# Performance work log

Measured on AMD Instinct MI355X. Metric: run time of the kernel, lower is better.

## Reference

```python
import jax, jax.numpy as jnp
import numpy as np

N = 1024      # n_nodes
S = 32        # state_dim
M = 32        # message_dim
STEPS = 5     # n_steps


def setup_inputs() -> dict:
    key = jax.random.key(0)
    ks = jax.random.split(key, 12)
    w = lambda k, shape: jax.random.normal(k, shape, jnp.float32) * 0.02
    return {
        "J": jax.random.normal(ks[0], (N, N), jnp.float32),
        "b": jax.random.normal(ks[1], (N,), jnp.float32),
        # message_passing MLP (Linear(2S+3->M), Linear(M->M), Linear(M->M))
        "W1": w(ks[2], (M, 2 * S + 3)), "b1": jnp.zeros((M,), jnp.float32),
        "W2": w(ks[3], (M, M)),         "b2": jnp.zeros((M,), jnp.float32),
        "W3": w(ks[4], (M, M)),         "b3": jnp.zeros((M,), jnp.float32),
        # GRU(input=S+M, hidden=S). h0 is always zero in the original forward,
        # so weight_hh never contributes (only bias_hh does) and is omitted.
        "W_ih": w(ks[5], (3 * S, S + M)),
        "b_ih": w(ks[6], (3 * S,)),
        "b_hh": w(ks[7], (3 * S,)),
        # readout MLP (Linear(S->M), Linear(M->M), Linear(M->2))
        "R1": w(ks[8], (M, S)),  "rb1": jnp.zeros((M,), jnp.float32),
        "R2": w(ks[9], (M, M)),  "rb2": jnp.zeros((M,), jnp.float32),
        "R3": w(ks[10], (2, M)), "rb3": jnp.zeros((2,), jnp.float32),
    }


def reference(J, b, W1, b1, W2, b2, W3, b3, W_ih, b_ih, b_hh, R1, rb1, R2, rb2, R3, rb3):
    # Split first linear over the concat [h_i, h_j, J_ij, b_i, b_j] so the
    # [N, N, 2S+3] concat tensor is never materialized.
    W1a, W1b = W1[:, :S], W1[:, S:2 * S]
    wJ, wbi, wbj = W1[:, 2 * S], W1[:, 2 * S + 1], W1[:, 2 * S + 2]

    def step(h, _):
        hi = h @ W1a.T                       # [N, M] (sender part)
        hj = h @ W1b.T                       # [N, M] (receiver part)
        pre = (hi[:, None, :] + hj[None, :, :]
               + J[:, :, None] * wJ
               + b[:, None, None] * wbi
               + b[None, :, None] * wbj
               + b1)                          # [N, N, M]
        x = jax.nn.relu(pre)
        x = jax.nn.relu(x @ W2.T + b2)
        x = jax.nn.relu(x @ W3.T + b3)       # message_i_j: [N, N, M]
        m = x.sum(0)                          # message to node j: sum over senders i
        # GRU with zero initial hidden state: h' = (1-z) * n_gate
        gi = jnp.concatenate([h, m], axis=-1) @ W_ih.T + b_ih  # [N, 3S]
        r = jax.nn.sigmoid(gi[:, :S] + b_hh[:S])
        z = jax.nn.sigmoid(gi[:, S:2 * S] + b_hh[S:2 * S])
        n = jnp.tanh(gi[:, 2 * S:] + r * b_hh[2 * S:])
        return (1.0 - z) * n, None

    h0 = jnp.zeros((N, S), J.dtype)
    h, _ = jax.lax.scan(step, h0, None, length=STEPS)

    r = jax.nn.relu(h @ R1.T + rb1)
    r = jax.nn.relu(r @ R2.T + rb2)
    r = jax.nn.relu(r @ R3.T + rb3)          # [N, 2]
    return jax.nn.sigmoid(r)
```

## Files before the change

### kernel.cpp

```cpp
#include <hip/hip_runtime.h>
#include <math.h>

#define NN 1024

typedef __attribute__((ext_vector_type(8))) short bf16x8;
typedef __attribute__((ext_vector_type(4))) float f32x4;
typedef __attribute__((ext_vector_type(2))) float f32x2;
typedef __attribute__((ext_vector_type(4))) unsigned int u32x4;

__device__ __forceinline__ float sigmoidf_(float x) { return 1.0f / (1.0f + __expf(-x)); }

__device__ __forceinline__ unsigned int pk2(float a, float b) {
    return __builtin_amdgcn_perm(__float_as_uint(a) + 0x8000u,
                                 __float_as_uint(b) + 0x8000u, 0x03020706u);
}
__device__ __forceinline__ unsigned int pkcvt(float a, float b) {
#if __has_builtin(__builtin_amdgcn_cvt_pk_bf16_f32)
    return __builtin_bit_cast(unsigned int, __builtin_amdgcn_cvt_pk_bf16_f32(a, b));
#else
    return pk2(a, b);
#endif
}
__device__ __forceinline__ unsigned short f2bf_rne(float a) {
    unsigned int ua = __float_as_uint(a);
    ua += 0x7fffu + ((ua >> 16) & 1u);
    return (unsigned short)(ua >> 16);
}

#define CFG_FLOATS 2560

__global__ __launch_bounds__(256) void k_pre(
    const float* __restrict__ J, const float* __restrict__ b,
    const float* __restrict__ W1, const float* __restrict__ b1,
    const float* __restrict__ W2, const float* __restrict__ b2,
    const float* __restrict__ W3, const float* __restrict__ b3,
    float* __restrict__ Jt, float* __restrict__ h,
    float* __restrict__ u0, float* __restrict__ v, float* __restrict__ cfg)
{
    __shared__ float tile[32][33];
    const int t = blockIdx.x;
    const int tid = threadIdx.x;
    if (t < 1024) {
        int tx = (t & 31) * 32, ty = (t >> 5) * 32;
        int x = tid & 31, y = tid >> 5;
#pragma unroll
        for (int r = 0; r < 4; r++)
            tile[y + 8 * r][x] = J[(size_t)(ty + y + 8 * r) * NN + tx + x];
        __syncthreads();
#pragma unroll
        for (int r = 0; r < 4; r++)
            Jt[(size_t)(tx + y + 8 * r) * NN + ty + x] = tile[x][y + 8 * r];
    } else if (t < 1152) {
        int idx = (t - 1024) * 256 + tid;
        int row = idx >> 5, mm = idx & 31;
        float bi = b[row];
        h[idx]  = 0.f;
        u0[idx] = bi * W1[mm * 67 + 65];
        v[idx]  = fmaf(bi, W1[mm * 67 + 66], b1[mm]);
    } else if (tid < 64) {
        const int l = tid, p = l & 15, q = l >> 4;
        union FU { unsigned int d[4]; unsigned short s[8]; } t0, t1, t2, t3;
        float wj[8];
#pragma unroll
        for (int jj = 0; jj < 8; jj++) {
            int k = q * 8 + jj;
            t0.s[jj] = f2bf_rne(W2[p * 32 + k]);
            t1.s[jj] = f2bf_rne(W2[(16 + p) * 32 + k]);
            t2.s[jj] = f2bf_rne(W3[p * 32 + k]);
            t3.s[jj] = f2bf_rne(W3[(16 + p) * 32 + k]);
            wj[jj] = W1[k * 67 + 64];
        }
        u32x4* cw = (u32x4*)cfg;
        cw[l]       = *(u32x4*)t0.d;
        cw[64 + l]  = *(u32x4*)t1.d;
        cw[128 + l] = *(u32x4*)t2.d;
        cw[192 + l] = *(u32x4*)t3.d;
        f32x4* cf = (f32x4*)(cfg + 1024);
        f32x4 v0, v1, v2, v3;
#pragma unroll
        for (int r = 0; r < 4; r++) {
            v0[r] = b2[q * 4 + r];  v1[r] = b2[16 + q * 4 + r];
            v2[r] = b3[q * 4 + r];  v3[r] = b3[16 + q * 4 + r];
        }
        cf[l] = v0; cf[64 + l] = v1; cf[128 + l] = v2; cf[192 + l] = v3;
        f32x4* cj = (f32x4*)(cfg + 2048);
        f32x4 wlo, whi;
#pragma unroll
        for (int r = 0; r < 4; r++) { wlo[r] = wj[r]; whi[r] = wj[4 + r]; }
        cj[l] = wlo; cj[64 + l] = whi;
    }
}

__device__ __forceinline__ void tile_body(
    float jw, const float4& ua_c, const float4& ub_c,
    const f32x2* vv2, const f32x2* wj2,
    const bf16x8& w2a0, const bf16x8& w2a1,
    const bf16x8& w3a0, const bf16x8& w3a1,
    const f32x4& b2v0, const f32x4& b2v1,
    const f32x4& b3v0, const f32x4& b3v1,
    int s0, int s1, bool qlo, f32x4& acc0, f32x4& acc1)
{
    const f32x2 jw2 = {jw, jw};
    const f32x2 z2 = {0.f, 0.f};
    const f32x4 z4 = {0.f, 0.f, 0.f, 0.f};

    f32x2 x0 = {ua_c.x, ua_c.y}, x1 = {ua_c.z, ua_c.w};
    f32x2 x2 = {ub_c.x, ub_c.y}, x3 = {ub_c.z, ub_c.w};
    x0 = jw2 * wj2[0] + (x0 + vv2[0]);
    x1 = jw2 * wj2[1] + (x1 + vv2[1]);
    x2 = jw2 * wj2[2] + (x2 + vv2[2]);
    x3 = jw2 * wj2[3] + (x3 + vv2[3]);
    x0 = __builtin_elementwise_max(x0, z2);
    x1 = __builtin_elementwise_max(x1, z2);
    x2 = __builtin_elementwise_max(x2, z2);
    x3 = __builtin_elementwise_max(x3, z2);

    union BU { u32x4 u4; bf16x8 v; unsigned int d[4]; } bx;
    bx.d[0] = pkcvt(x0[0], x0[1]);
    bx.d[1] = pkcvt(x1[0], x1[1]);
    bx.d[2] = pkcvt(x2[0], x2[1]);
    bx.d[3] = pkcvt(x3[0], x3[1]);

    f32x4 c0 = __builtin_amdgcn_mfma_f32_16x16x32_bf16(w2a0, bx.v, b2v0, 0, 0, 0);
    f32x4 c1 = __builtin_amdgcn_mfma_f32_16x16x32_bf16(w2a1, bx.v, b2v1, 0, 0, 0);
    c0 = __builtin_elementwise_max(c0, z4);
    c1 = __builtin_elementwise_max(c1, z4);

    const int d0 = (int)pkcvt(c0[0], c0[1]);
    const int d1 = (int)pkcvt(c0[2], c0[3]);
    const int d2 = (int)pkcvt(c1[0], c1[1]);
    const int d3 = (int)pkcvt(c1[2], c1[3]);

    const int A0 = __builtin_amdgcn_ds_bpermute(s0, d0);
    const int A1 = __builtin_amdgcn_ds_bpermute(s0, d1);
    const int A2 = __builtin_amdgcn_ds_bpermute(s1, d0);
    const int A3 = __builtin_amdgcn_ds_bpermute(s1, d1);
    const int B0 = __builtin_amdgcn_ds_bpermute(s0, d2);
    const int B1 = __builtin_amdgcn_ds_bpermute(s0, d3);
    const int B2 = __builtin_amdgcn_ds_bpermute(s1, d2);
    const int B3 = __builtin_amdgcn_ds_bpermute(s1, d3);

    union BU yr;
    yr.d[0] = (unsigned)(qlo ? A0 : B0);
    yr.d[1] = (unsigned)(qlo ? A1 : B1);
    yr.d[2] = (unsigned)(qlo ? A2 : B2);
    yr.d[3] = (unsigned)(qlo ? A3 : B3);

    f32x4 e0 = __builtin_amdgcn_mfma_f32_16x16x32_bf16(w3a0, yr.v, b3v0, 0, 0, 0);
    f32x4 e1 = __builtin_amdgcn_mfma_f32_16x16x32_bf16(w3a1, yr.v, b3v1, 0, 0, 0);
    acc0 = acc0 + __builtin_elementwise_max(e0, z4);
    acc1 = acc1 + __builtin_elementwise_max(e1, z4);
}

__global__ __launch_bounds__(256, 4) void k_main(
    const float* __restrict__ Jt, const float* __restrict__ cfg,
    const float* __restrict__ v, const float* __restrict__ ui,
    float* __restrict__ mpart)
{
    __shared__ float red[4 * 32];
    const int tid = threadIdx.x;
    const int w = tid >> 6;
    const int l = tid & 63;
    const int p = l & 15;
    const int q = l >> 4;
    const int j = blockIdx.x >> 1;
    const int half = blockIdx.x & 1;

    union FU { bf16x8 v; u32x4 u4; } w2a0, w2a1, w3a0, w3a1;
    const u32x4* cw = (const u32x4*)cfg;
    w2a0.u4 = cw[l]; w2a1.u4 = cw[64 + l]; w3a0.u4 = cw[128 + l]; w3a1.u4 = cw[192 + l];
    const f32x4* cf = (const f32x4*)(cfg + 1024);
    const f32x4 b2v0 = cf[l], b2v1 = cf[64 + l], b3v0 = cf[128 + l], b3v1 = cf[192 + l];
    const f32x4* cj = (const f32x4*)(cfg + 2048);
    const f32x4 wlo = cj[l], whi = cj[64 + l];
    f32x2 wj2[4] = { {wlo[0], wlo[1]}, {wlo[2], wlo[3]}, {whi[0], whi[1]}, {whi[2], whi[3]} };

    f32x2 vv2[4];
    {
        float4 va = *(const float4*)(v + j * 32 + q * 8);
        float4 vb = *(const float4*)(v + j * 32 + q * 8 + 4);
        vv2[0] = f32x2{va.x, va.y}; vv2[1] = f32x2{va.z, va.w};
        vv2[2] = f32x2{vb.x, vb.y}; vv2[3] = f32x2{vb.z, vb.w};
    }

    const float* Jtrow = Jt + (size_t)j * NN;
    const int s0 = (p | ((l & 16) << 1)) << 2;
    const int s1 = s0 + 64;
    const bool qlo = (l & 32) == 0;

    f32x4 acc0 = {0.f, 0.f, 0.f, 0.f}, acc1 = {0.f, 0.f, 0.f, 0.f};

    const int ibase = half * 512 + w * 128;
    int iA = ibase + p, iB = ibase + 16 + p;
    float  jwA = Jtrow[iA];
    float4 uaA = *(const float4*)(ui + iA * 32 + q * 8);
    float4 ubA = *(const float4*)(ui + iA * 32 + q * 8 + 4);
    float  jwB = Jtrow[iB];
    float4 uaB = *(const float4*)(ui + iB * 32 + q * 8);
    float4 ubB = *(const float4*)(ui + iB * 32 + q * 8 + 4);

#pragma unroll
    for (int tt = 0; tt < 4; ++tt) {
        const float  jwA_c = jwA; const float4 uaA_c = uaA, ubA_c = ubA;
        const float  jwB_c = jwB; const float4 uaB_c = uaB, ubB_c = ubB;
        if (tt < 3) {
            const int inA = ibase + (2 * tt + 2) * 16 + p;
            const int inB = inA + 16;
            jwA = Jtrow[inA];
            uaA = *(const float4*)(ui + inA * 32 + q * 8);
            ubA = *(const float4*)(ui + inA * 32 + q * 8 + 4);
            jwB = Jtrow[inB];
            uaB = *(const float4*)(ui + inB * 32 + q * 8);
            ubB = *(const float4*)(ui + inB * 32 + q * 8 + 4);
        }
        tile_body(jwA_c, uaA_c, ubA_c, vv2, wj2, w2a0.v, w2a1.v, w3a0.v, w3a1.v,
                  b2v0, b2v1, b3v0, b3v1, s0, s1, qlo, acc0, acc1);
        tile_body(jwB_c, uaB_c, ubB_c, vv2, wj2, w2a0.v, w2a1.v, w3a0.v, w3a1.v,
                  b2v0, b2v1, b3v0, b3v1, s0, s1, qlo, acc0, acc1);
    }

#pragma unroll
    for (int bit = 1; bit < 16; bit <<= 1) {
#pragma unroll
        for (int r = 0; r < 4; r++) {
            acc0[r] += __shfl_xor(acc0[r], bit);
            acc1[r] += __shfl_xor(acc1[r], bit);
        }
    }
    if (p == 0) {
#pragma unroll
        for (int r = 0; r < 4; r++) {
            red[w * 32 + q * 4 + r]      = acc0[r];
            red[w * 32 + 16 + q * 4 + r] = acc1[r];
        }
    }
    __syncthreads();
    if (tid < 32)
        mpart[(half << 15) + j * 32 + tid] =
            red[tid] + red[32 + tid] + red[64 + tid] + red[96 + tid];
}

__global__ __launch_bounds__(256) void k_tail(
    const float* __restrict__ Wih, const float* __restrict__ bih,
    const float* __restrict__ bhh, const float* __restrict__ b,
    const float* __restrict__ b1, const float* __restrict__ W1,
    const float* __restrict__ R1, const float* __restrict__ rb1,
    const float* __restrict__ R2, const float* __restrict__ rb2,
    const float* __restrict__ R3, const float* __restrict__ rb3,
    float* __restrict__ h, float* __restrict__ v,
    const float* __restrict__ mpart, float* __restrict__ uo,
    float* __restrict__ out, int do_out)
{
    __shared__ float hm[64], gbuf[96], hnb[32], tb[32];
    const int tid = threadIdx.x;
    const int j = blockIdx.x;

    if (tid < 64) {
        float val;
        if (tid < 32) val = h[j * 32 + tid];
        else {
            int s = tid - 32;
            val = mpart[j * 32 + s] + mpart[32768 + j * 32 + s];
        }
        hm[tid] = val;
    }
    __syncthreads();

    if (tid < 192) {
        const int row = tid >> 1, half = tid & 1;
        const float* wr = Wih + row * 64 + half * 32;
        const float* hh = hm + half * 32;
        float acc = 0.f;
#pragma unroll
        for (int k4 = 0; k4 < 8; k4++) {
            float4 w4 = *(const float4*)(wr + 4 * k4);
            acc = fmaf(w4.x, hh[4 * k4 + 0], acc);
            acc = fmaf(w4.y, hh[4 * k4 + 1], acc);
            acc = fmaf(w4.z, hh[4 * k4 + 2], acc);
            acc = fmaf(w4.w, hh[4 * k4 + 3], acc);
        }
        acc += __shfl_xor(acc, 1);
        if (half == 0) gbuf[row] = acc + bih[row];
    }
    __syncthreads();

    if (tid < 32) {
        const int s = tid;
        float r = sigmoidf_(gbuf[s] + bhh[s]);
        float z = sigmoidf_(gbuf[32 + s] + bhh[32 + s]);
        float n = tanhf(gbuf[64 + s] + r * bhh[64 + s]);
        float hn_ = (1.0f - z) * n;
        hnb[s] = hn_;
        h[j * 32 + s] = hn_;
    }
    __syncthreads();

    if (tid < 64) {
        const int s = tid & 31;
        const bool isV = tid >= 32;
        const float bj = b[j];
        const float* wr = W1 + s * 67 + (isV ? 32 : 0);
        float acc = isV ? fmaf(bj, W1[s * 67 + 66], b1[s]) : bj * W1[s * 67 + 65];
#pragma unroll
        for (int k = 0; k < 32; k++) acc = fmaf(wr[k], hnb[k], acc);
        if (isV) v[j * 32 + s] = acc;
        else     uo[j * 32 + s] = acc;
    }

    if (do_out) {
        __syncthreads();
        if (tid < 32) {
            float a = rb1[tid];
            const float* rr = R1 + tid * 32;
#pragma unroll 8
            for (int k = 0; k < 32; k++) a = fmaf(rr[k], hnb[k], a);
            gbuf[tid] = fmaxf(a, 0.f);
        }
        __syncthreads();
        if (tid < 32) {
            float a = rb2[tid];
            const float* rr = R2 + tid * 32;
#pragma unroll 8
            for (int k = 0; k < 32; k++) a = fmaf(rr[k], gbuf[k], a);
            tb[tid] = fmaxf(a, 0.f);
        }
        __syncthreads();
        if (tid < 2) {
            float a = rb3[tid];
            const float* rr = R3 + tid * 32;
#pragma unroll 8
            for (int k = 0; k < 32; k++) a = fmaf(rr[k], tb[k], a);
            out[j * 2 + tid] = sigmoidf_(fmaxf(a, 0.f));
        }
    }
}

extern "C" void kernel_launch(void* const* d_in, const int* in_sizes, int n_in,
                              void* d_out, int out_size, void* d_ws, size_t ws_size,
                              hipStream_t stream)
{
    const float* J   = (const float*)d_in[0];
    const float* b   = (const float*)d_in[1];
    const float* W1  = (const float*)d_in[2];
    const float* b1  = (const float*)d_in[3];
    const float* W2  = (const float*)d_in[4];
    const float* b2  = (const float*)d_in[5];
    const float* W3  = (const float*)d_in[6];
    const float* b3  = (const float*)d_in[7];
    const float* Wih = (const float*)d_in[8];
    const float* bih = (const float*)d_in[9];
    const float* bhh = (const float*)d_in[10];
    const float* R1  = (const float*)d_in[11];
    const float* rb1 = (const float*)d_in[12];
    const float* R2  = (const float*)d_in[13];
    const float* rb2 = (const float*)d_in[14];
    const float* R3  = (const float*)d_in[15];
    const float* rb3 = (const float*)d_in[16];

    float* out = (float*)d_out;
    float* ws  = (float*)d_ws;
    float* h     = ws;
    float* v     = ws + 32768;
    float* u0    = ws + 65536;
    float* u1    = ws + 98304;
    float* Jt    = ws + 131072;
    float* cfg   = ws + 131072 + NN * NN;
    float* mpart = cfg + CFG_FLOATS;

    k_pre<<<1153, 256, 0, stream>>>(J, b, W1, b1, W2, b2, W3, b3,
                                    Jt, h, u0, v, cfg);
    for (int s = 0; s < 5; s++) {
        const float* ui = (s & 1) ? u1 : u0;
        float*       uo = (s & 1) ? u0 : u1;
        k_main<<<2048, 256, 0, stream>>>(Jt, cfg, v, ui, mpart);
        k_tail<<<1024, 256, 0, stream>>>(Wih, bih, bhh, b, b1, W1,
                                         R1, rb1, R2, rb2, R3, rb3,
                                         h, v, mpart, uo, out, (s == 4) ? 1 : 0);
    }
}
```

Measured before the change: 229.4 us.

## Fuse message kernel and GRU tail into one per-step kernel

Merges k_main and k_tail into a single k_step kernel. Each block now handles one receiver node j across all 1024 senders, instead of two blocks splitting the senders in half. The partial message sum is reduced in shared memory and fed straight into the GRU/readout tail. This removes the mpart global round-trip and one kernel launch per step. In exchange, the grid is halved to 1024 blocks and each block runs a longer serial loop, which lowers parallelism.

Result: faster. 202.0 us (-12.0%).

```diff
diff --git a/kernel.cpp b/kernel.cpp
--- a/kernel.cpp
+++ b/kernel.cpp
@@ -152,19 +152,27 @@
     acc1 = acc1 + __builtin_elementwise_max(e1, z4);
 }
 
-__global__ __launch_bounds__(256, 4) void k_main(
+__global__ __launch_bounds__(256, 4) void k_step(
     const float* __restrict__ Jt, const float* __restrict__ cfg,
-    const float* __restrict__ v, const float* __restrict__ ui,
-    float* __restrict__ mpart)
+    const float* __restrict__ Wih, const float* __restrict__ bih,
+    const float* __restrict__ bhh, const float* __restrict__ b,
+    const float* __restrict__ b1, const float* __restrict__ W1,
+    const float* __restrict__ R1, const float* __restrict__ rb1,
+    const float* __restrict__ R2, const float* __restrict__ rb2,
+    const float* __restrict__ R3, const float* __restrict__ rb3,
+    float* __restrict__ h, float* __restrict__ v,
+    const float* __restrict__ ui, float* __restrict__ uo,
+    float* __restrict__ out, int do_out)
 {
     __shared__ float red[4 * 32];
+    __shared__ float hm[64], gbuf[96], hnb[32], tb[32];
+
     const int tid = threadIdx.x;
     const int w = tid >> 6;
     const int l = tid & 63;
     const int p = l & 15;
     const int q = l >> 4;
-    const int j = blockIdx.x >> 1;
-    const int half = blockIdx.x & 1;
+    const int j = blockIdx.x;
 
     union FU { bf16x8 v; u32x4 u4; } w2a0, w2a1, w3a0, w3a1;
     const u32x4* cw = (const u32x4*)cfg;
@@ -183,35 +191,34 @@
         vv2[2] = f32x2{vb.x, vb.y}; vv2[3] = f32x2{vb.z, vb.w};
     }
 
-    const float* Jtrow = Jt + (size_t)j * NN;
     const int s0 = (p | ((l & 16) << 1)) << 2;
     const int s1 = s0 + 64;
     const bool qlo = (l & 32) == 0;
 
     f32x4 acc0 = {0.f, 0.f, 0.f, 0.f}, acc1 = {0.f, 0.f, 0.f, 0.f};
 
-    const int ibase = half * 512 + w * 128;
-    int iA = ibase + p, iB = ibase + 16 + p;
-    float  jwA = Jtrow[iA];
-    float4 uaA = *(const float4*)(ui + iA * 32 + q * 8);
-    float4 ubA = *(const float4*)(ui + iA * 32 + q * 8 + 4);
-    float  jwB = Jtrow[iB];
-    float4 uaB = *(const float4*)(ui + iB * 32 + q * 8);
-    float4 ubB = *(const float4*)(ui + iB * 32 + q * 8 + 4);
-
-#pragma unroll
-    for (int tt = 0; tt < 4; ++tt) {
+    const int ibase = w * 256;
+    const float* jp = Jt + (size_t)j * NN + ibase + p;
+    const float* up = ui + (size_t)(ibase + p) * 32 + q * 8;
+
+    float  jwA = jp[0],  jwB = jp[16];
+    float4 uaA = *(const float4*)(up);
+    float4 ubA = *(const float4*)(up + 4);
+    float4 uaB = *(const float4*)(up + 512);
+    float4 ubB = *(const float4*)(up + 516);
+
+#pragma unroll
+    for (int tt = 0; tt < 8; ++tt) {
         const float  jwA_c = jwA; const float4 uaA_c = uaA, ubA_c = ubA;
         const float  jwB_c = jwB; const float4 uaB_c = uaB, ubB_c = ubB;
-        if (tt < 3) {
-            const int inA = ibase + (2 * tt + 2) * 16 + p;
-            const int inB = inA + 16;
-            jwA = Jtrow[inA];
-            uaA = *(const float4*)(ui + inA * 32 + q * 8);
-            ubA = *(const float4*)(ui + inA * 32 + q * 8 + 4);
-            jwB = Jtrow[inB];
-            uaB = *(const float4*)(ui + inB * 32 + q * 8);
-            ubB = *(const float4*)(ui + inB * 32 + q * 8 + 4);
+        if (tt < 7) {
+            const float* jn = jp + (tt + 1) * 32;
+            const float* un = up + (size_t)(tt + 1) * 1024;
+            jwA = jn[0];  jwB = jn[16];
+            uaA = *(const float4*)(un);
+            ubA = *(const float4*)(un + 4);
+            uaB = *(const float4*)(un + 512);
+            ubB = *(const float4*)(un + 516);
         }
         tile_body(jwA_c, uaA_c, ubA_c, vv2, wj2, w2a0.v, w2a1.v, w3a0.v, w3a1.v,
                   b2v0, b2v1, b3v0, b3v1, s0, s1, qlo, acc0, acc1);
@@ -235,32 +242,13 @@
         }
     }
     __syncthreads();
-    if (tid < 32)
-        mpart[(half << 15) + j * 32 + tid] =
-            red[tid] + red[32 + tid] + red[64 + tid] + red[96 + tid];
-}
-
-__global__ __launch_bounds__(256) void k_tail(
-    const float* __restrict__ Wih, const float* __restrict__ bih,
-    const float* __restrict__ bhh, const float* __restrict__ b,
-    const float* __restrict__ b1, const float* __restrict__ W1,
-    const float* __restrict__ R1, const float* __restrict__ rb1,
-    const float* __restrict__ R2, const float* __restrict__ rb2,
-    const float* __restrict__ R3, const float* __restrict__ rb3,
-    float* __restrict__ h, float* __restrict__ v,
-    const float* __restrict__ mpart, float* __restrict__ uo,
-    float* __restrict__ out, int do_out)
-{
-    __shared__ float hm[64], gbuf[96], hnb[32], tb[32];
-    const int tid = threadIdx.x;
-    const int j = blockIdx.x;
 
     if (tid < 64) {
         float val;
         if (tid < 32) val = h[j * 32 + tid];
         else {
             int s = tid - 32;
-            val = mpart[j * 32 + s] + mpart[32768 + j * 32 + s];
+            val = red[s] + red[32 + s] + red[64 + s] + red[96 + s];
         }
         hm[tid] = val;
     }
@@ -359,22 +347,20 @@
 
     float* out = (float*)d_out;
     float* ws  = (float*)d_ws;
-    float* h     = ws;
-    float* v     = ws + 32768;
-    float* u0    = ws + 65536;
-    float* u1    = ws + 98304;
-    float* Jt    = ws + 131072;
-    float* cfg   = ws + 131072 + NN * NN;
-    float* mpart = cfg + CFG_FLOATS;
+    float* h   = ws;
+    float* v   = ws + 32768;
+    float* u0  = ws + 65536;
+    float* u1  = ws + 98304;
+    float* Jt  = ws + 131072;
+    float* cfg = ws + 131072 + NN * NN;
 
     k_pre<<<1153, 256, 0, stream>>>(J, b, W1, b1, W2, b2, W3, b3,
                                     Jt, h, u0, v, cfg);
     for (int s = 0; s < 5; s++) {
         const float* ui = (s & 1) ? u1 : u0;
         float*       uo = (s & 1) ? u0 : u1;
-        k_main<<<2048, 256, 0, stream>>>(Jt, cfg, v, ui, mpart);
-        k_tail<<<1024, 256, 0, stream>>>(Wih, bih, bhh, b, b1, W1,
+        k_step<<<1024, 256, 0, stream>>>(Jt, cfg, Wih, bih, bhh, b, b1, W1,
                                          R1, rb1, R2, rb2, R3, rb3,
-                                         h, v, mpart, uo, out, (s == 4) ? 1 : 0);
-    }
-}
+                                         h, v, ui, uo, out, (s == 4) ? 1 : 0);
+    }
+}
```
